# Kernel optimization log

Hardware: AMD Instinct MI355X
Metric: run time of the kernel (lower is better)

The kernel has to match this reference:

```python
import jax, jax.numpy as jnp
import numpy as np

N_HEAD = 16
D_HEAD = 64
LN_EPS = 1e-5


def _layernorm(x, g, b):
    mu = jnp.mean(x, axis=-1, keepdims=True)
    var = jnp.mean((x - mu) ** 2, axis=-1, keepdims=True)
    return (x - mu) * jax.lax.rsqrt(var + LN_EPS) * g + b


def setup_inputs() -> dict:
    key = jax.random.key(0)
    ks = jax.random.split(key, 10)
    n_token, d_model, d_inner, n_layer = 32000, 1024, 4096, 6
    qlen, mlen, bsz = 512, 512, 4
    s = 0.02
    return {
        'data': jax.random.randint(ks[0], (qlen, bsz), 0, n_token),
        'mems': jax.random.normal(ks[1], (n_layer, mlen, bsz, d_model), jnp.float32) * s,
        'emb': jax.random.normal(ks[2], (n_token, d_model), jnp.float32) * s,
        'Wq': jax.random.normal(ks[3], (n_layer, d_model, N_HEAD * D_HEAD), jnp.float32) * s,
        'Wkv': jax.random.normal(ks[4], (n_layer, d_model, 2 * N_HEAD * D_HEAD), jnp.float32) * s,
        'Wo': jax.random.normal(ks[5], (n_layer, N_HEAD * D_HEAD, d_model), jnp.float32) * s,
        'ln1_g': jnp.ones((n_layer, d_model), jnp.float32),
        'ln1_b': jnp.zeros((n_layer, d_model), jnp.float32),
        'W1': jax.random.normal(ks[6], (n_layer, d_model, d_inner), jnp.float32) * s,
        'b1': jnp.zeros((n_layer, d_inner), jnp.float32),
        'W2': jax.random.normal(ks[7], (n_layer, d_inner, d_model), jnp.float32) * s,
        'b2': jnp.zeros((n_layer, d_model), jnp.float32),
        'ln2_g': jnp.ones((n_layer, d_model), jnp.float32),
        'ln2_b': jnp.zeros((n_layer, d_model), jnp.float32),
    }


def reference(data, mems, emb, Wq, Wkv, Wo, ln1_g, ln1_b, W1, b1, W2, b2, ln2_g, ln2_b):
    qlen, bsz = data.shape
    n_layer, _, d_model = Wo.shape
    mlen = mems.shape[1]
    klen = mlen + qlen
    scale = 1.0 / np.sqrt(D_HEAD)

    # AdaptiveEmbedding (div_val=1, d_proj==d_embed): lookup * sqrt(d_proj)
    word_emb = emb[data] * np.sqrt(d_model)  # [q, b, d]

    # sinusoidal positional embedding over klen (attn_type=2), last qlen slice
    inv_freq = 1.0 / (10000.0 ** (jnp.arange(0, d_model, 2, dtype=jnp.float32) / d_model))
    pos_seq = jnp.arange(klen - 1, -1, -1, dtype=jnp.float32)
    sinu = pos_seq[:, None] * inv_freq[None, :]
    pos_emb = jnp.concatenate([jnp.sin(sinu), jnp.cos(sinu)], axis=-1)  # [klen, d]
    h = word_emb + pos_emb[-qlen:, None, :]

    # causal mask including memory: True = masked
    mask = jnp.triu(jnp.ones((qlen, klen), dtype=bool), k=1 + mlen)

    for l in range(n_layer):
        c = jnp.concatenate([mems[l], h], axis=0)  # [klen, b, d]
        q = (h @ Wq[l]).reshape(qlen, bsz, N_HEAD, D_HEAD)
        kv = (c @ Wkv[l]).reshape(klen, bsz, N_HEAD, 2 * D_HEAD)
        k, v = kv[..., :D_HEAD], kv[..., D_HEAD:]
        score = jnp.einsum('ibnd,jbnd->ijbn', q, k) * scale  # [q, klen, b, n]
        score = jnp.where(mask[:, :, None, None], -jnp.inf, score)
        prob = jax.nn.softmax(score, axis=1)
        attn_vec = jnp.einsum('ijbn,jbnd->ibnd', prob, v).reshape(qlen, bsz, N_HEAD * D_HEAD)
        h = _layernorm(h + attn_vec @ Wo[l], ln1_g[l], ln1_b[l])  # post-LN
        ff = jax.nn.relu(h @ W1[l] + b1[l]) @ W2[l] + b2[l]
        h = _layernorm(h + ff, ln2_g[l], ln2_b[l])
    return h
```

## Files before the change

kernel.cpp:

```cpp
#include <hip/hip_runtime.h>

typedef unsigned short u16;
typedef unsigned int u32;
typedef __bf16 bf16x8 __attribute__((ext_vector_type(8)));
typedef float f32x4 __attribute__((ext_vector_type(4)));
typedef u16 u16x8 __attribute__((ext_vector_type(8)));
typedef u16 u16x4 __attribute__((ext_vector_type(4)));
typedef u32 u32x4 __attribute__((ext_vector_type(4)));

__device__ __forceinline__ u16 f2bf(float f){
  unsigned u = __float_as_uint(f);
  u += 0x7FFFu + ((u >> 16) & 1u);
  return (u16)(u >> 16);
}
__device__ __forceinline__ float bf2f(u16 u){
  return __uint_as_float((u32)u << 16);
}
__device__ __forceinline__ u32 pack2bf(float a, float b){
  return (u32)f2bf(a) | ((u32)f2bf(b) << 16);
}
__device__ __forceinline__ void gload16(const void* g, void* l){
  __builtin_amdgcn_global_load_lds(
      (const __attribute__((address_space(1))) void*)g,
      (__attribute__((address_space(3))) void*)l, 16, 0, 0);
}

__global__ __launch_bounds__(256) void conv_bf16_t(const float* __restrict__ src, u16* __restrict__ dst,
                                                   int K, int N, size_t dls, int drow0){
  __shared__ u16 s[64 * 68];
  size_t lo = (size_t)blockIdx.z * K * N;
  int n0 = blockIdx.x << 6, k0 = blockIdx.y << 6;
  int t = threadIdx.x;
#pragma unroll
  for (int p = 0; p < 4; ++p){
    int idx = p * 1024 + t * 4;
    int kl = idx >> 6, nl = idx & 63;
    f32x4 v = *(const f32x4*)(src + lo + (size_t)(k0 + kl) * N + n0 + nl);
#pragma unroll
    for (int j = 0; j < 4; ++j) s[(nl + j) * 68 + kl] = f2bf(v[j]);
  }
  __syncthreads();
  u16* db = dst + blockIdx.z * dls;
#pragma unroll
  for (int p = 0; p < 4; ++p){
    int idx = p * 1024 + t * 4;
    int nl = idx >> 6, kl = idx & 63;
    u16x4 o;
#pragma unroll
    for (int j = 0; j < 4; ++j) o[j] = s[nl * 68 + kl + j];
    *(u16x4*)(db + (size_t)(drow0 + n0 + nl) * K + k0 + kl) = o;
  }
}

__global__ __launch_bounds__(256) void conv_bf16(const float* __restrict__ src, u16* __restrict__ dst){
  size_t i = ((size_t)blockIdx.x * 256 + threadIdx.x) * 4;
  f32x4 v = *(const f32x4*)(src + i);
  u16x4 o;
#pragma unroll
  for (int j = 0; j < 4; ++j) o[j] = f2bf(v[j]);
  *(u16x4*)(dst + i) = o;
}

__global__ __launch_bounds__(256) void embed_k(const int* __restrict__ data, const float* __restrict__ emb,
                                               u16* __restrict__ hbf){
  int idx = blockIdx.x * 256 + threadIdx.x;
  int r = idx >> 10, d = idx & 1023;
  int i = r >> 2;
  int e = data[r];
  float val = emb[(size_t)e * 1024 + d] * 32.0f;
  float pos = (float)(511 - i);
  int t = d & 511;
  float freq = powf(10000.0f, -(float)t * (1.0f / 512.0f));
  float ang = pos * freq;
  val += (d < 512) ? sinf(ang) : cosf(ang);
  hbf[idx] = f2bf(val);
}

template<int BM>
__global__ __launch_bounds__(256) void gemm_bt(
    const u16* __restrict__ A, const u16* __restrict__ Bt,
    const float* __restrict__ bias, float* __restrict__ C, u16* __restrict__ Cbf,
    u16* __restrict__ Cpart, int M, int N, int K, int kchunk, int relu,
    size_t zA, size_t zB, size_t zC,
    u16* __restrict__ VT, size_t zVT, int vcol0, int jdst0)
{
  constexpr int MFR = BM / 32;
  constexpr int ASZ = BM * 64, BSZ = 128 * 64;
  __shared__ __align__(16) u16 sA[2 * ASZ];
  __shared__ __align__(16) u16 sB[2 * BSZ];
  int tid = threadIdx.x, lane = tid & 63;
  int wr = (tid >> 7) & 1, wc = (tid >> 6) & 1;

  u32 gx = gridDim.x, gy = gridDim.y;
  u32 flat = blockIdx.x + gx * (blockIdx.y + gy * blockIdx.z);
  u32 chunk = (gx * gy * gridDim.z) >> 3;
  u32 swz = (flat & 7) * chunk + (flat >> 3);
  u32 bx = swz % gx, rest = swz / gx;
  u32 by = rest % gy, bz = rest / gy;

  int m0 = by * BM, n0 = bx << 7;
  int z = bz;
  int kbeg = Cpart ? z * kchunk : 0;

  const u16* Ap = A + (size_t)z * zA;
  const u16* Bp = Bt + (size_t)z * zB;

  f32x4 acc[MFR][4];
#pragma unroll
  for (int i = 0; i < MFR; ++i)
#pragma unroll
    for (int j = 0; j < 4; ++j) acc[i][j] = (f32x4)(0.0f);

  int srow8 = tid >> 3;
  int gslot8 = ((tid & 7) ^ (srow8 & 7)) << 3;
  const u16* Ab = Ap + (size_t)(m0 + srow8) * K + kbeg + gslot8;
  const u16* Bb = Bp + (size_t)(n0 + srow8) * K + kbeg + gslot8;
  const size_t rstep32 = (size_t)K << 5;

  auto stage = [&](int buf, int k0){
#pragma unroll
    for (int p = 0; p < BM / 32; ++p)
      gload16(Ab + p * rstep32 + k0, (void*)&sA[buf * ASZ + p * 2048 + tid * 8]);
#pragma unroll
    for (int p = 0; p < 4; ++p)
      gload16(Bb + p * rstep32 + k0, (void*)&sB[buf * BSZ + p * 2048 + tid * 8]);
  };

  int r15 = lane & 15, g = lane >> 4;
  int s0 = g ^ (r15 & 7);
  const int o0 = s0 * 8, o1 = (s0 ^ 4) * 8;
  const int paBase = (wr * (BM / 2) + r15) * 64;
  const int pbBase = (wc * 64 + r15) * 64;

  int nk = kchunk >> 6;
  stage(0, 0);
  __syncthreads();
  for (int t = 0; t < nk; ++t){
    int cur = t & 1;
    if (t + 1 < nk) stage(cur ^ 1, (t + 1) << 6);
    const u16* pa = sA + cur * ASZ;
    const u16* pb = sB + cur * BSZ;
    bf16x8 af[MFR][2], bfv[4][2];
#pragma unroll
    for (int mi = 0; mi < MFR; ++mi){
      af[mi][0] = *(const bf16x8*)(pa + paBase + mi * 1024 + o0);
      af[mi][1] = *(const bf16x8*)(pa + paBase + mi * 1024 + o1);
    }
#pragma unroll
    for (int ni = 0; ni < 4; ++ni){
      bfv[ni][0] = *(const bf16x8*)(pb + pbBase + ni * 1024 + o0);
      bfv[ni][1] = *(const bf16x8*)(pb + pbBase + ni * 1024 + o1);
    }
#pragma unroll
    for (int kk = 0; kk < 2; ++kk)
#pragma unroll
      for (int mi = 0; mi < MFR; ++mi)
#pragma unroll
        for (int ni = 0; ni < 4; ++ni)
          acc[mi][ni] = __builtin_amdgcn_mfma_f32_16x16x32_bf16(af[mi][kk], bfv[ni][kk], acc[mi][ni], 0, 0, 0);
    __syncthreads();
  }

  int colf = lane & 15, rowf = (lane >> 4) << 2;
  bool vtile = (VT != nullptr) && (n0 >= vcol0);
  if (Cpart){
    u16* dst = Cpart + (size_t)z * M * N;
#pragma unroll
    for (int ni = 0; ni < 4; ++ni){
      int cg = n0 + (wc << 6) + ni * 16 + colf;
#pragma unroll
      for (int mi = 0; mi < MFR; ++mi){
        int rg = m0 + wr * (BM / 2) + mi * 16 + rowf;
#pragma unroll
        for (int r = 0; r < 4; ++r)
          dst[(size_t)(rg + r) * N + cg] = f2bf(acc[mi][ni][r]);
      }
    }
  } else {
    if (!(vtile && wc == 1)){
#pragma unroll
      for (int ni = 0; ni < 4; ++ni){
        int cg = n0 + (wc << 6) + ni * 16 + colf;
        float bv = bias ? bias[cg] : 0.0f;
#pragma unroll
        for (int mi = 0; mi < MFR; ++mi){
          int rg = m0 + wr * (BM / 2) + mi * 16 + rowf;
#pragma unroll
          for (int r = 0; r < 4; ++r){
            float val = acc[mi][ni][r] + bv;
            if (relu) val = fmaxf(val, 0.0f);
            size_t o = (size_t)(rg + r) * N + cg;
            if (C)   C[o]   = val;
            if (Cbf) (Cbf + (size_t)z * zC)[o] = f2bf(val);
          }
        }
      }
    }
    if (vtile){
      if (wc == 1){
#pragma unroll
        for (int ni = 0; ni < 4; ++ni)
#pragma unroll
          for (int mi = 0; mi < MFR; ++mi)
#pragma unroll
            for (int r = 0; r < 4; ++r)
              sA[(wr * (BM / 2) + mi * 16 + rowf + r) * 68 + ni * 16 + colf] = f2bf(acc[mi][ni][r]);
      }
      __syncthreads();
      int vb = tid >> 6, vd = tid & 63;
      int nh = (n0 - vcol0) >> 7;
      u16* dst = VT + (size_t)z * zVT + (((size_t)((vb << 4) + nh) << 6) + vd) * 1024 + jdst0 + (m0 >> 2);
      u16 tmp[BM / 4];
#pragma unroll
      for (int jj = 0; jj < BM / 4; ++jj) tmp[jj] = sA[((jj << 2) + vb) * 68 + vd];
#pragma unroll
      for (int c = 0; c < BM / 32; ++c)
        *(u16x8*)(dst + c * 8) = *(const u16x8*)(&tmp[c * 8]);
    }
  }
}

__global__ __launch_bounds__(256) void attn_mfma(
    const u16* __restrict__ qkv, const u16* __restrict__ kvm,
    const u16* __restrict__ vtbf, u16* __restrict__ attnbf)
{
  __shared__ __align__(16) u16 sK[4][64 * 64];
  __shared__ __align__(16) u16 sV[4][64 * 64];
  int tid = threadIdx.x, lane = tid & 63, wid = tid >> 6;
  int g = lane >> 4, t = lane & 15;

  u32 flat = blockIdx.x + (blockIdx.y << 3);
  u32 swz = (flat & 7) * 64 + (flat >> 3);
  int qt = swz & 7, bnp = swz >> 3;

  int b = bnp >> 4, n = bnp & 15;
  int i0 = qt * 64 + wid * 16;
  int i = i0 + t;

  union Cvt { u32x4 u; bf16x8 v; };

  bf16x8 qfrag[2];
#pragma unroll
  for (int ks = 0; ks < 2; ++ks)
    qfrag[ks] = *(const bf16x8*)(qkv + (size_t)(i * 4 + b) * 3072 + n * 64 + ks * 32 + g * 8);

  f32x4 oacc[4];
#pragma unroll
  for (int df = 0; df < 4; ++df) oacc[df] = (f32x4)(0.0f);
  float mrun = -1e30f, lrun = 0.0f;

  const u16* kbm = kvm + n * 128;
  const u16* kbh = qkv + 1024 + n * 128;
  const u16* vb2 = vtbf + ((size_t)bnp << 16);

  int srow = tid >> 3;
  int gsl = ((tid & 7) ^ (srow & 7)) << 3;

  auto stageKV = [&](int buf, int kt){
    int j0 = kt << 6;
    const u16* kb = (kt < 8) ? kbm : kbh;
    size_t kst = (kt < 8) ? 2048 : 3072;
    int joff = (kt < 8) ? 0 : 512;
#pragma unroll
    for (int p = 0; p < 2; ++p){
      int jl = srow + p * 32;
      gload16(kb + (size_t)((j0 + jl - joff) * 4 + b) * kst + gsl, (void*)&sK[buf][p * 2048 + tid * 8]);
    }
#pragma unroll
    for (int p = 0; p < 2; ++p){
      int dl = srow + p * 32;
      gload16(vb2 + ((size_t)dl << 10) + j0 + gsl, (void*)&sV[buf][p * 2048 + tid * 8]);
    }
  };

  auto compute = [&](int cur, int kt){
    int j0 = kt << 6;
    f32x4 sacc[4];
#pragma unroll
    for (int jf = 0; jf < 4; ++jf) sacc[jf] = (f32x4)(0.0f);
    __builtin_amdgcn_s_setprio(1);
#pragma unroll
    for (int ks = 0; ks < 2; ++ks){
      int sl = ((ks * 4 + g) ^ (t & 7)) * 8;
#pragma unroll
      for (int jf = 0; jf < 4; ++jf){
        bf16x8 kf = *(const bf16x8*)(&sK[cur][(jf * 16 + t) * 64 + sl]);
        sacc[jf] = __builtin_amdgcn_mfma_f32_16x16x32_bf16(kf, qfrag[ks], sacc[jf], 0, 0, 0);
      }
    }
    __builtin_amdgcn_s_setprio(0);
    bool part = (j0 + 63 > i0 + 512);
    float ps[4][4];
    float tmax = -1e30f;
#pragma unroll
    for (int jf = 0; jf < 4; ++jf)
#pragma unroll
      for (int r = 0; r < 4; ++r){
        float s = sacc[jf][r] * 0.125f;
        if (part && (j0 + jf * 16 + g * 4 + r > i + 512)) s = -1e30f;
        ps[jf][r] = s;
        tmax = fmaxf(tmax, s);
      }
    tmax = fmaxf(tmax, __shfl_xor(tmax, 16));
    tmax = fmaxf(tmax, __shfl_xor(tmax, 32));
    float mnew = fmaxf(mrun, tmax);
    float sc = __expf(mrun - mnew);
    mrun = mnew;
    lrun *= sc;
    u32 pk0[2], pk1[2], pk2[2], pk3[2];
    {
      float e0, e1, e2, e3;
#define DO_JF(PK, JF) \
      e0 = __expf(ps[JF][0] - mnew); e1 = __expf(ps[JF][1] - mnew); \
      e2 = __expf(ps[JF][2] - mnew); e3 = __expf(ps[JF][3] - mnew); \
      lrun += (e0 + e1) + (e2 + e3); \
      PK[0] = pack2bf(e0, e1); PK[1] = pack2bf(e2, e3);
      DO_JF(pk0, 0) DO_JF(pk1, 1) DO_JF(pk2, 2) DO_JF(pk3, 3)
#undef DO_JF
    }
#pragma unroll
    for (int df = 0; df < 4; ++df)
#pragma unroll
      for (int r = 0; r < 4; ++r) oacc[df][r] *= sc;

    int srcA = t + 16 * ((2 * g) & 3);
    int srcB = t + 16 * ((2 * g + 1) & 3);
    bool ghi = (g >= 2);
#pragma unroll
    for (int ks = 0; ks < 2; ++ks){
      u32 w0a, w1a, w2a, w3a, w0b, w1b, w2b, w3b;
      if (ks == 0){
        w0a = __shfl((int)pk0[0], srcA); w1a = __shfl((int)pk0[1], srcA);
        w2a = __shfl((int)pk0[0], srcB); w3a = __shfl((int)pk0[1], srcB);
        w0b = __shfl((int)pk1[0], srcA); w1b = __shfl((int)pk1[1], srcA);
        w2b = __shfl((int)pk1[0], srcB); w3b = __shfl((int)pk1[1], srcB);
      } else {
        w0a = __shfl((int)pk2[0], srcA); w1a = __shfl((int)pk2[1], srcA);
        w2a = __shfl((int)pk2[0], srcB); w3a = __shfl((int)pk2[1], srcB);
        w0b = __shfl((int)pk3[0], srcA); w1b = __shfl((int)pk3[1], srcA);
        w2b = __shfl((int)pk3[0], srcB); w3b = __shfl((int)pk3[1], srcB);
      }
      Cvt c;
      c.u[0] = ghi ? w0b : w0a;
      c.u[1] = ghi ? w1b : w1a;
      c.u[2] = ghi ? w2b : w2a;
      c.u[3] = ghi ? w3b : w3a;
      bf16x8 pf = c.v;
      int sl = ((ks * 4 + g) ^ (t & 7)) * 8;
      __builtin_amdgcn_s_setprio(1);
#pragma unroll
      for (int df = 0; df < 4; ++df){
        bf16x8 vf = *(const bf16x8*)(&sV[cur][(df * 16 + t) * 64 + sl]);
        oacc[df] = __builtin_amdgcn_mfma_f32_16x16x32_bf16(vf, pf, oacc[df], 0, 0, 0);
      }
      __builtin_amdgcn_s_setprio(0);
    }
  };

  int kt1 = qt + 9;
  stageKV(0, 0);
  stageKV(1, 1);
  __syncthreads();
  for (int kt = 0; kt < kt1; kt += 2){
    if (kt + 2 < kt1) stageKV((kt + 2) & 3, kt + 2);
    if (kt + 3 < kt1) stageKV((kt + 3) & 3, kt + 3);
    compute(kt & 3, kt);
    if (kt + 1 < kt1) compute((kt + 1) & 3, kt + 1);
    __syncthreads();
  }
  lrun += __shfl_xor(lrun, 16);
  lrun += __shfl_xor(lrun, 32);
  float inv = 1.0f / lrun;

  u16* orow = attnbf + ((size_t)(i * 4 + b) << 10) + n * 64;
#pragma unroll
  for (int df = 0; df < 4; ++df){
#pragma unroll
    for (int h = 0; h < 2; ++h){
      *(u32*)(orow + df * 16 + g * 4 + 2 * h) = pack2bf(oacc[df][2 * h] * inv, oacc[df][2 * h + 1] * inv);
    }
  }
}

__global__ __launch_bounds__(256) void ln_k(const u16* __restrict__ resbf, const u16* __restrict__ parts,
                                            size_t pstride, int np, const float* __restrict__ bias,
                                            const float* __restrict__ g, const float* __restrict__ bta,
                                            u16* __restrict__ hbf, float* __restrict__ fout)
{
  int row = blockIdx.x, tid = threadIdx.x;
  int d0 = tid << 2;
  size_t ro = (size_t)row << 10;
  u16x4 rv = *(const u16x4*)(resbf + ro + d0);
  f32x4 v;
#pragma unroll
  for (int j = 0; j < 4; ++j) v[j] = bf2f(rv[j]);
  if (bias){
    f32x4 bv = *(const f32x4*)(bias + d0);
#pragma unroll
    for (int j = 0; j < 4; ++j) v[j] += bv[j];
  }
  for (int p = 0; p < np; ++p){
    u16x4 pv = *(const u16x4*)(parts + p * pstride + ro + d0);
#pragma unroll
    for (int j = 0; j < 4; ++j) v[j] += bf2f(pv[j]);
  }
  float s = (v[0] + v[1]) + (v[2] + v[3]);
  float s2 = (v[0] * v[0] + v[1] * v[1]) + (v[2] * v[2] + v[3] * v[3]);
#pragma unroll
  for (int off = 32; off; off >>= 1){ s += __shfl_xor(s, off); s2 += __shfl_xor(s2, off); }
  __shared__ float ps[8];
  int wid = tid >> 6, lane = tid & 63;
  if (lane == 0){ ps[wid] = s; ps[wid + 4] = s2; }
  __syncthreads();
  s  = ps[0] + ps[1] + ps[2] + ps[3];
  s2 = ps[4] + ps[5] + ps[6] + ps[7];
  float mu = s * 0.0009765625f;
  float var = s2 * 0.0009765625f - mu * mu;
  float rstd = rsqrtf(var + 1e-5f);
  f32x4 gv = *(const f32x4*)(g + d0);
  f32x4 bt = *(const f32x4*)(bta + d0);
  f32x4 fo;
  u16x4 hb;
#pragma unroll
  for (int j = 0; j < 4; ++j){
    float tv = (v[j] - mu) * rstd * gv[j] + bt[j];
    fo[j] = tv; hb[j] = f2bf(tv);
  }
  *(u16x4*)(hbf + ro + d0) = hb;
  if (fout) *(f32x4*)(fout + ro + d0) = fo;
}

extern "C" void kernel_launch(void* const* d_in, const int* in_sizes, int n_in,
                              void* d_out, int out_size, void* d_ws, size_t ws_size,
                              hipStream_t stream)
{
  const int*   data = (const int*)  d_in[0];
  const float* mems = (const float*)d_in[1];
  const float* emb  = (const float*)d_in[2];
  const float* Wq   = (const float*)d_in[3];
  const float* Wkv  = (const float*)d_in[4];
  const float* Wo   = (const float*)d_in[5];
  const float* ln1g = (const float*)d_in[6];
  const float* ln1b = (const float*)d_in[7];
  const float* W1   = (const float*)d_in[8];
  const float* b1   = (const float*)d_in[9];
  const float* W2   = (const float*)d_in[10];
  const float* b2   = (const float*)d_in[11];
  const float* ln2g = (const float*)d_in[12];
  const float* ln2b = (const float*)d_in[13];
  float* out = (float*)d_out;

  char* ws = (char*)d_ws;
  size_t off = 0;
  auto alloc = [&](size_t bytes) -> char* {
    char* p = ws + off;
    off = (off + bytes + 255) & ~(size_t)255;
    return p;
  };

  u16*   wqkv_bf = (u16*) alloc((size_t)6 * 3072 * 1024 * 2);
  u16*   wo_bf   = (u16*) alloc((size_t)6 * 1024 * 1024 * 2);
  u16*   w1_bf   = (u16*) alloc((size_t)6 * 4096 * 1024 * 2);
  u16*   w2_bf   = (u16*) alloc((size_t)6 * 1024 * 4096 * 2);
  u16*   memsbf  = (u16*) alloc((size_t)6 * 2048 * 1024 * 2);
  u16*   kvmem   = (u16*) alloc((size_t)6 * 2048 * 2048 * 2);
  u16*   vtbf    = (u16*) alloc((size_t)6 * 64 * 64 * 1024 * 2);
  u16*   hbf     = (u16*) alloc((size_t)2048 * 1024 * 2);
  u16*   qkv     = (u16*) alloc((size_t)2048 * 3072 * 2);
  u16*   attnbf  = (u16*) alloc((size_t)2048 * 1024 * 2);
  u16*   f1bf    = (u16*) alloc((size_t)2048 * 4096 * 2);
  u16*   pbf     = (u16*) alloc((size_t)4 * 2048 * 1024 * 2);
  const size_t PS = (size_t)2048 * 1024;
  const size_t VTL = (size_t)64 * 64 * 1024;

  conv_bf16_t<<<dim3(16, 16, 6), 256, 0, stream>>>(Wq,  wqkv_bf, 1024, 1024, (size_t)3072 * 1024, 0);
  conv_bf16_t<<<dim3(32, 16, 6), 256, 0, stream>>>(Wkv, wqkv_bf, 1024, 2048, (size_t)3072 * 1024, 1024);
  conv_bf16_t<<<dim3(16, 16, 6), 256, 0, stream>>>(Wo,  wo_bf,   1024, 1024, (size_t)1024 * 1024, 0);
  conv_bf16_t<<<dim3(64, 16, 6), 256, 0, stream>>>(W1,  w1_bf,   1024, 4096, (size_t)4096 * 1024, 0);
  conv_bf16_t<<<dim3(16, 64, 6), 256, 0, stream>>>(W2,  w2_bf,   4096, 1024, (size_t)4096 * 1024, 0);
  conv_bf16<<<12288, 256, 0, stream>>>(mems, memsbf);
  embed_k<<<8192, 256, 0, stream>>>(data, emb, hbf);
  gemm_bt<128><<<dim3(16, 16, 6), 256, 0, stream>>>(memsbf, wqkv_bf + (size_t)1024 * 1024, nullptr,
      nullptr, kvmem, nullptr, 2048, 2048, 1024, 1024, 0,
      (size_t)2048 * 1024, (size_t)3072 * 1024, (size_t)2048 * 2048,
      vtbf, VTL, 0, 0);

  for (int l = 0; l < 6; ++l){
    u16* kvm_l = kvmem + (size_t)l * 2048 * 2048;
    u16* vt_l  = vtbf + (size_t)l * VTL;
    gemm_bt<64><<<dim3(24, 32), 256, 0, stream>>>(hbf, wqkv_bf + (size_t)l * 3072 * 1024, nullptr,
        nullptr, qkv, nullptr, 2048, 3072, 1024, 1024, 0, 0, 0, 0,
        vt_l, 0, 1024, 512);
    attn_mfma<<<dim3(8, 64), 256, 0, stream>>>(qkv, kvm_l, vt_l, attnbf);
    gemm_bt<64><<<dim3(8, 32, 2), 256, 0, stream>>>(attnbf, wo_bf + (size_t)l * 1024 * 1024, nullptr,
        nullptr, nullptr, pbf, 2048, 1024, 1024, 512, 0, 0, 0, 0,
        nullptr, 0, 0, 0);
    ln_k<<<2048, 256, 0, stream>>>(hbf, pbf, PS, 2, nullptr, ln1g + l * 1024, ln1b + l * 1024, hbf, nullptr);
    gemm_bt<128><<<dim3(32, 16), 256, 0, stream>>>(hbf, w1_bf + (size_t)l * 4096 * 1024,
        b1 + (size_t)l * 4096, nullptr, f1bf, nullptr, 2048, 4096, 1024, 1024, 1, 0, 0, 0,
        nullptr, 0, 0, 0);
    gemm_bt<128><<<dim3(8, 16, 4), 256, 0, stream>>>(f1bf, w2_bf + (size_t)l * 4096 * 1024, nullptr,
        nullptr, nullptr, pbf, 2048, 1024, 4096, 1024, 0, 0, 0, 0,
        nullptr, 0, 0, 0);
    ln_k<<<2048, 256, 0, stream>>>(hbf, pbf, PS, 4, b2 + l * 1024, ln2g + l * 1024, ln2b + l * 1024,
                                   hbf, (l == 5) ? out : nullptr);
  }
}
```

Baseline: 987.1 us.

## Add dedicated 256x128-tile triple-buffered GEMM kernel for the FFN W1 projection

Replaces the generic gemm_bt<128> launch for the W1+bias+ReLU layer with a new 512-thread kernel using 256x128 output tiles, triple-buffered LDS staging via global_load_lds, and loads interleaved between MFMA groups with s_setprio. Larger tiles raise operand reuse per LDS load and halve the grid, and the three-stage pipeline aims to hide global latency. Risks include higher LDS use (144 KB) limiting occupancy to one block per CU, fewer blocks (256) relative to CU count, and an uncoalesced scalar epilogue store of bf16 outputs.

```diff
diff --git a/kernel.cpp b/kernel.cpp
--- a/kernel.cpp
+++ b/kernel.cpp
@@ -216,6 +216,154 @@
 #pragma unroll
       for (int c = 0; c < BM / 32; ++c)
         *(u16x8*)(dst + c * 8) = *(const u16x8*)(&tmp[c * 8]);
+    }
+  }
+}
+
+__global__ __launch_bounds__(512) void gemm_w1(
+    const u16* __restrict__ A, const u16* __restrict__ Bt,
+    const float* __restrict__ bias, u16* __restrict__ Cbf, int N, int K, int relu)
+{
+  __shared__ __align__(16) u16 sA[3][256 * 64];
+  __shared__ __align__(16) u16 sB[3][128 * 64];
+  int tid = threadIdx.x, lane = tid & 63, wid = tid >> 6;
+  int wr = wid >> 1, wc = wid & 1;
+
+  u32 gx = gridDim.x;
+  u32 flat = blockIdx.x + gx * blockIdx.y;
+  u32 chunk = (gx * gridDim.y) >> 3;
+  u32 swz = (flat & 7) * chunk + (flat >> 3);
+  u32 bx = swz % gx, by = swz / gx;
+  int n0 = bx << 7, m0 = by << 8;
+
+  f32x4 acc[4][4];
+#pragma unroll
+  for (int i = 0; i < 4; ++i)
+#pragma unroll
+    for (int j = 0; j < 4; ++j) acc[i][j] = (f32x4)(0.0f);
+
+  int srow = tid >> 3;
+  int gslot = ((tid & 7) ^ (srow & 7)) << 3;
+  const u16* Ab = A + (size_t)(m0 + srow) * K + gslot;
+  const u16* Bb = Bt + (size_t)(n0 + srow) * K + gslot;
+  const size_t r64 = (size_t)K << 6;
+
+  auto stageA01 = [&](int buf, int kt){ int k0 = kt << 6;
+    gload16(Ab + k0,           (void*)&sA[buf][tid * 8]);
+    gload16(Ab + r64 + k0,     (void*)&sA[buf][4096 + tid * 8]); };
+  auto stageA23 = [&](int buf, int kt){ int k0 = kt << 6;
+    gload16(Ab + 2 * r64 + k0, (void*)&sA[buf][8192 + tid * 8]);
+    gload16(Ab + 3 * r64 + k0, (void*)&sA[buf][12288 + tid * 8]); };
+  auto stageB   = [&](int buf, int kt){ int k0 = kt << 6;
+    gload16(Bb + k0,           (void*)&sB[buf][tid * 8]);
+    gload16(Bb + r64 + k0,     (void*)&sB[buf][4096 + tid * 8]); };
+
+  int r15 = lane & 15, g = lane >> 4;
+  int s0 = g ^ (r15 & 7);
+  const int o0 = s0 * 8, o1 = (s0 ^ 4) * 8;
+  const int aBase = (wr * 64 + r15) * 64;
+  const int bBase = (wc * 64 + r15) * 64;
+
+  int nu = K >> 6;
+  stageA01(0, 0); stageA23(0, 0); stageB(0, 0);
+  stageA01(1, 1); stageA23(1, 1); stageB(1, 1);
+  asm volatile("s_waitcnt vmcnt(6)" ::: "memory");
+  __builtin_amdgcn_s_barrier();
+
+  for (int u = 0; u < nu; ++u){
+    int cb = u % 3, nb = (u + 2) % 3;
+    bool pf = (u + 2 < nu);
+    const u16* pa = &sA[cb][0];
+    const u16* pb = &sB[cb][0];
+    bf16x8 af[2][2], bf[2][2];
+    if (pf) stageA01(nb, u + 2);
+#pragma unroll
+    for (int mi = 0; mi < 2; ++mi){
+      af[mi][0] = *(const bf16x8*)(pa + aBase + mi * 1024 + o0);
+      af[mi][1] = *(const bf16x8*)(pa + aBase + mi * 1024 + o1);
+    }
+#pragma unroll
+    for (int ni = 0; ni < 2; ++ni){
+      bf[ni][0] = *(const bf16x8*)(pb + bBase + ni * 1024 + o0);
+      bf[ni][1] = *(const bf16x8*)(pb + bBase + ni * 1024 + o1);
+    }
+    __builtin_amdgcn_s_setprio(1);
+#pragma unroll
+    for (int mi = 0; mi < 2; ++mi)
+#pragma unroll
+      for (int ni = 0; ni < 2; ++ni){
+        acc[mi][ni] = __builtin_amdgcn_mfma_f32_16x16x32_bf16(af[mi][0], bf[ni][0], acc[mi][ni], 0, 0, 0);
+        acc[mi][ni] = __builtin_amdgcn_mfma_f32_16x16x32_bf16(af[mi][1], bf[ni][1], acc[mi][ni], 0, 0, 0);
+      }
+    __builtin_amdgcn_s_setprio(0);
+    if (pf) stageA23(nb, u + 2);
+#pragma unroll
+    for (int ni = 0; ni < 2; ++ni){
+      bf[ni][0] = *(const bf16x8*)(pb + bBase + 2048 + ni * 1024 + o0);
+      bf[ni][1] = *(const bf16x8*)(pb + bBase + 2048 + ni * 1024 + o1);
+    }
+    __builtin_amdgcn_s_setprio(1);
+#pragma unroll
+    for (int mi = 0; mi < 2; ++mi)
+#pragma unroll
+      for (int ni = 0; ni < 2; ++ni){
+        acc[mi][ni + 2] = __builtin_amdgcn_mfma_f32_16x16x32_bf16(af[mi][0], bf[ni][0], acc[mi][ni + 2], 0, 0, 0);
+        acc[mi][ni + 2] = __builtin_amdgcn_mfma_f32_16x16x32_bf16(af[mi][1], bf[ni][1], acc[mi][ni + 2], 0, 0, 0);
+      }
+    __builtin_amdgcn_s_setprio(0);
+    if (pf) stageB(nb, u + 2);
+#pragma unroll
+    for (int mi = 0; mi < 2; ++mi){
+      af[mi][0] = *(const bf16x8*)(pa + aBase + 2048 + mi * 1024 + o0);
+      af[mi][1] = *(const bf16x8*)(pa + aBase + 2048 + mi * 1024 + o1);
+    }
+#pragma unroll
+    for (int ni = 0; ni < 2; ++ni){
+      bf[ni][0] = *(const bf16x8*)(pb + bBase + ni * 1024 + o0);
+      bf[ni][1] = *(const bf16x8*)(pb + bBase + ni * 1024 + o1);
+    }
+    __builtin_amdgcn_s_setprio(1);
+#pragma unroll
+    for (int mi = 0; mi < 2; ++mi)
+#pragma unroll
+      for (int ni = 0; ni < 2; ++ni){
+        acc[mi + 2][ni] = __builtin_amdgcn_mfma_f32_16x16x32_bf16(af[mi][0], bf[ni][0], acc[mi + 2][ni], 0, 0, 0);
+        acc[mi + 2][ni] = __builtin_amdgcn_mfma_f32_16x16x32_bf16(af[mi][1], bf[ni][1], acc[mi + 2][ni], 0, 0, 0);
+      }
+    __builtin_amdgcn_s_setprio(0);
+#pragma unroll
+    for (int ni = 0; ni < 2; ++ni){
+      bf[ni][0] = *(const bf16x8*)(pb + bBase + 2048 + ni * 1024 + o0);
+      bf[ni][1] = *(const bf16x8*)(pb + bBase + 2048 + ni * 1024 + o1);
+    }
+    __builtin_amdgcn_s_setprio(1);
+#pragma unroll
+    for (int mi = 0; mi < 2; ++mi)
+#pragma unroll
+      for (int ni = 0; ni < 2; ++ni){
+        acc[mi + 2][ni + 2] = __builtin_amdgcn_mfma_f32_16x16x32_bf16(af[mi][0], bf[ni][0], acc[mi + 2][ni + 2], 0, 0, 0);
+        acc[mi + 2][ni + 2] = __builtin_amdgcn_mfma_f32_16x16x32_bf16(af[mi][1], bf[ni][1], acc[mi + 2][ni + 2], 0, 0, 0);
+      }
+    __builtin_amdgcn_s_setprio(0);
+    if (u + 2 < nu)      { asm volatile("s_waitcnt vmcnt(6)" ::: "memory"); }
+    else if (u + 1 < nu) { asm volatile("s_waitcnt vmcnt(0)" ::: "memory"); }
+    __builtin_amdgcn_s_barrier();
+  }
+
+  int colf = lane & 15, rowf = (lane >> 4) << 2;
+#pragma unroll
+  for (int ni = 0; ni < 4; ++ni){
+    int cg = n0 + wc * 64 + ni * 16 + colf;
+    float bv = bias ? bias[cg] : 0.0f;
+#pragma unroll
+    for (int mi = 0; mi < 4; ++mi){
+      int rg = m0 + wr * 64 + mi * 16 + rowf;
+#pragma unroll
+      for (int r = 0; r < 4; ++r){
+        float val = acc[mi][ni][r] + bv;
+        if (relu) val = fmaxf(val, 0.0f);
+        Cbf[(size_t)(rg + r) * N + cg] = f2bf(val);
+      }
     }
   }
 }
@@ -496,9 +644,8 @@
         nullptr, nullptr, pbf, 2048, 1024, 1024, 512, 0, 0, 0, 0,
         nullptr, 0, 0, 0);
     ln_k<<<2048, 256, 0, stream>>>(hbf, pbf, PS, 2, nullptr, ln1g + l * 1024, ln1b + l * 1024, hbf, nullptr);
-    gemm_bt<128><<<dim3(32, 16), 256, 0, stream>>>(hbf, w1_bf + (size_t)l * 4096 * 1024,
-        b1 + (size_t)l * 4096, nullptr, f1bf, nullptr, 2048, 4096, 1024, 1024, 1, 0, 0, 0,
-        nullptr, 0, 0, 0);
+    gemm_w1<<<dim3(32, 8), 512, 0, stream>>>(hbf, w1_bf + (size_t)l * 4096 * 1024,
+        b1 + (size_t)l * 4096, f1bf, 4096, 1024, 1);
     gemm_bt<128><<<dim3(8, 16, 4), 256, 0, stream>>>(f1bf, w2_bf + (size_t)l * 4096 * 1024, nullptr,
         nullptr, nullptr, pbf, 2048, 1024, 4096, 1024, 0, 0, 0, 0,
         nullptr, 0, 0, 0);
```

Result: slower. 1.013 ms (+2.7%).
